# Performance work log

Measured on AMD Instinct MI355X. Metric: run time of the kernel, lower is better.

## Reference

```python
import jax, jax.numpy as jnp
import numpy as np

EPS_COS = 1e-8
EPS_NORM = 1e-12
LN_EPS = 1e-5
OT_REG = 0.05
OT_ITERS = 5

B, L, D_IN, D_H = 16, 512, 1024, 1024


def setup_inputs() -> dict:
    key = jax.random.key(0)
    ks = jax.random.split(key, 16)
    p = lambda k, shape: 0.02 * jax.random.normal(k, shape, dtype=jnp.float32)
    return {
        "origin_seq": jax.random.normal(ks[0], (B, L, D_IN), dtype=jnp.float32),
        "target_seq": jax.random.normal(ks[1], (B, L, D_IN), dtype=jnp.float32),
        "W_ori": p(ks[2], (D_IN, D_H)), "b_ori": jnp.zeros((D_H,), jnp.float32),
        "W_tar": p(ks[3], (D_IN, D_H)), "b_tar": jnp.zeros((D_H,), jnp.float32),
        "W_ft": p(ks[4], (D_H, D_H)), "b_ft": jnp.zeros((D_H,), jnp.float32),
        "W_fo": p(ks[5], (D_H, D_H)), "b_fo": jnp.zeros((D_H,), jnp.float32),
        "W_fot": p(ks[6], (D_H, D_H)), "b_fot": jnp.zeros((D_H,), jnp.float32),
        "ln_g": jnp.ones((D_H,), jnp.float32), "ln_b": jnp.zeros((D_H,), jnp.float32),
    }


def _l2norm(x, eps):
    return x / jnp.maximum(jnp.linalg.norm(x, axis=-1, keepdims=True), eps)


def _forward(origin_seq, target_seq, W_ori, b_ori, W_tar, b_tar, W_ft, b_ft,
             W_fo, b_fo, W_fot, b_fot, ln_g, ln_b):
    ori = origin_seq @ W_ori + b_ori            # [B, Lo, H]
    tar = target_seq @ W_tar + b_tar            # [B, Lt, H]
    tar = tar @ W_ft + b_ft
    ori_fc = ori @ W_fo + b_fo
    ori_tp = ori @ W_fot + b_fot
    # cosine similarity cost: [B, Lt, Lo]
    C = jnp.einsum('bth,boh->bto', _l2norm(tar, EPS_COS), _l2norm(ori_fc, EPS_COS))
    # Sinkhorn: alternating row/col normalization of exp(C/eps)
    Q = jnp.exp(C / OT_REG)
    for _ in range(OT_ITERS):
        Q = Q / jnp.sum(Q, axis=-1, keepdims=True)
        Q = Q / jnp.sum(Q, axis=-2, keepdims=True)
    plan = _l2norm(Q, EPS_NORM)                 # F.normalize(dim=-1); dropout is eval no-op
    out = jnp.einsum('bto,boh->bth', plan, ori_tp) + tar
    mu = jnp.mean(out, axis=-1, keepdims=True)
    var = jnp.mean((out - mu) ** 2, axis=-1, keepdims=True)
    return ((out - mu) * jax.lax.rsqrt(var + LN_EPS)) * ln_g + ln_b


def reference(origin_seq, target_seq, W_ori, b_ori, W_tar, b_tar, W_ft, b_ft,
              W_fo, b_fo, W_fot, b_fot, ln_g, ln_b):
    return _forward(origin_seq, target_seq, W_ori, b_ori, W_tar, b_tar, W_ft, b_ft,
                    W_fo, b_fo, W_fot, b_fot, ln_g, ln_b)
```

## Files before the change

### kernel.cpp

```cpp
#include <hip/hip_runtime.h>
#include <hip/hip_bf16.h>
#include <math.h>

constexpr int Bn = 16;
constexpr int Ln = 512;
constexpr int Hn = 1024;
constexpr int RowsT = Bn * Ln;

typedef __attribute__((ext_vector_type(8))) short bf16x8;
typedef __attribute__((ext_vector_type(4))) float f32x4;
typedef __attribute__((ext_vector_type(8))) unsigned short u16x8;

__device__ __forceinline__ unsigned short f2bf(float f) {
  unsigned u = __float_as_uint(f);
  u += 0x7FFFu + ((u >> 16) & 1u);
  return (unsigned short)(u >> 16);
}
__device__ __forceinline__ float bf2f(unsigned short u) {
  return __uint_as_float(((unsigned)u) << 16);
}

__device__ __forceinline__ void gload_lds16(const void* g, void* l) {
  __builtin_amdgcn_global_load_lds(
      (const __attribute__((address_space(1))) void*)g,
      (__attribute__((address_space(3))) void*)l, 16, 0, 0);
}

__device__ __forceinline__ float block_reduce_sum(float v) {
  __shared__ float sbuf[8];
  const int lane = threadIdx.x & 63;
  const int wid = threadIdx.x >> 6;
#pragma unroll
  for (int off = 32; off > 0; off >>= 1) v += __shfl_down(v, off, 64);
  __syncthreads();
  if (lane == 0) sbuf[wid] = v;
  __syncthreads();
  if (threadIdx.x == 0) {
    float t = 0.f;
    const int nw = (blockDim.x + 63) >> 6;
    for (int i = 0; i < nw; ++i) t += sbuf[i];
    sbuf[0] = t;
  }
  __syncthreads();
  return sbuf[0];
}

__global__ __launch_bounds__(256) void conv_z(
    const float* __restrict__ s0, const float* __restrict__ s1,
    unsigned short* __restrict__ d0, unsigned short* __restrict__ d1) {
  const float* in = blockIdx.z ? s1 : s0;
  unsigned short* out = blockIdx.z ? d1 : d0;
  const size_t i = ((size_t)blockIdx.x * blockDim.x + threadIdx.x) * 8;
  const float4 a = *(const float4*)(in + i);
  const float4 b = *(const float4*)(in + i + 4);
  u16x8 r;
  r[0] = f2bf(a.x); r[1] = f2bf(a.y); r[2] = f2bf(a.z); r[3] = f2bf(a.w);
  r[4] = f2bf(b.x); r[5] = f2bf(b.y); r[6] = f2bf(b.z); r[7] = f2bf(b.w);
  *(u16x8*)(out + i) = r;
}

__global__ __launch_bounds__(256) void transpose_w_z(
    const float* __restrict__ s0, const float* __restrict__ s1,
    unsigned short* __restrict__ d0, unsigned short* __restrict__ d1,
    int K, int N) {
  const float* W = blockIdx.z ? s1 : s0;
  unsigned short* Wt = blockIdx.z ? d1 : d0;
  __shared__ float t[32][33];
  const int n0 = blockIdx.x * 32;
  const int k0 = blockIdx.y * 32;
  const int tx = threadIdx.x & 31;
  const int ty = threadIdx.x >> 5;
#pragma unroll
  for (int i = 0; i < 32; i += 8)
    t[ty + i][tx] = W[(size_t)(k0 + ty + i) * N + n0 + tx];
  __syncthreads();
#pragma unroll
  for (int i = 0; i < 32; i += 8)
    Wt[(size_t)(n0 + ty + i) * K + k0 + tx] = f2bf(t[tx][ty + i]);
}

__global__ __launch_bounds__(256) void bias_combine(
    const float* __restrict__ b1a, const float* __restrict__ Wa, const float* __restrict__ b2a,
    const float* __restrict__ b1b, const float* __restrict__ Wb, const float* __restrict__ b2b,
    const float* __restrict__ b1c, const float* __restrict__ Wc, const float* __restrict__ b2c,
    float* __restrict__ o0, float* __restrict__ o1, float* __restrict__ o2) {
  const int z = blockIdx.y;
  const float* b1 = z == 0 ? b1a : (z == 1 ? b1b : b1c);
  const float* W  = z == 0 ? Wa  : (z == 1 ? Wb  : Wc);
  const float* b2 = z == 0 ? b2a : (z == 1 ? b2b : b2c);
  float* out      = z == 0 ? o0  : (z == 1 ? o1  : o2);
  const int n = blockIdx.x * 256 + threadIdx.x;
  float s = b2[n];
  for (int j = 0; j < Hn; ++j) s += b1[j] * W[(size_t)j * Hn + n];
  out[n] = s;
}

#define MFMA_PROLOG(Aptr, Bptr, Kdim)                                          \
  constexpr int BK = 32;                                                       \
  __shared__ unsigned short As[128][BK];                                       \
  __shared__ unsigned short Bs[128][BK];                                       \
  const int tid = threadIdx.x;                                                 \
  const int wid = tid >> 6;                                                    \
  const int lane = tid & 63;                                                   \
  const int wr = (wid >> 1) * 64;                                              \
  const int wc = (wid & 1) * 64;                                               \
  const int sr = lane >> 2;                                                    \
  const int sk = (lane & 3) * 8;                                               \
  const size_t arow = (size_t)(row0 + wid * 32 + sr) * Kdim + sk;              \
  const size_t brow = (size_t)(col0 + wid * 32 + sr) * Kdim + sk;              \
  f32x4 acc[4][4] = {};                                                        \
  for (int k0 = 0; k0 < Kdim; k0 += BK) {                                      \
    gload_lds16(Aptr + arow + k0,                      &As[wid * 32][0]);      \
    gload_lds16(Aptr + arow + (size_t)16 * Kdim + k0,  &As[wid * 32 + 16][0]); \
    gload_lds16(Bptr + brow + k0,                      &Bs[wid * 32][0]);      \
    gload_lds16(Bptr + brow + (size_t)16 * Kdim + k0,  &Bs[wid * 32 + 16][0]); \
    __syncthreads();                                                           \
    bf16x8 af[4], bfr[4];                                                      \
    _Pragma("unroll")                                                          \
    for (int m = 0; m < 4; ++m)                                                \
      af[m] = *(const bf16x8*)&As[wr + m * 16 + (lane & 15)][(lane >> 4) * 8]; \
    _Pragma("unroll")                                                          \
    for (int n = 0; n < 4; ++n)                                                \
      bfr[n] = *(const bf16x8*)&Bs[wc + n * 16 + (lane & 15)][(lane >> 4) * 8];\
    _Pragma("unroll")                                                          \
    for (int m = 0; m < 4; ++m)                                                \
      _Pragma("unroll")                                                        \
      for (int n = 0; n < 4; ++n)                                              \
        acc[m][n] = __builtin_amdgcn_mfma_f32_16x16x32_bf16(af[m], bfr[n],     \
                                                            acc[m][n], 0, 0, 0);\
    __syncthreads();                                                           \
  }                                                                            \
  const int cr = (lane >> 4) * 4;                                              \
  const int cc = lane & 15;

__global__ __launch_bounds__(256) void mfma_gemm_z(
    const unsigned short* __restrict__ A0, const unsigned short* __restrict__ A1,
    const unsigned short* __restrict__ Bt0, const unsigned short* __restrict__ Bt1,
    const float* __restrict__ bias0, const float* __restrict__ bias1,
    unsigned short* __restrict__ D0, unsigned short* __restrict__ D1,
    int mode1, int N, int K) {
  const int z = blockIdx.z;
  const unsigned short* A = z ? A1 : A0;
  const unsigned short* Bt = z ? Bt1 : Bt0;
  const float* bias = z ? bias1 : bias0;
  unsigned short* D = z ? D1 : D0;
  const int mode = z ? mode1 : 0;
  const int row0 = blockIdx.y * 128;
  const int col0 = blockIdx.x * 128;
  MFMA_PROLOG(A, Bt, K)
  if (mode == 0) {
#pragma unroll
    for (int m = 0; m < 4; ++m) {
#pragma unroll
      for (int n = 0; n < 4; ++n) {
        const int gc = col0 + wc + n * 16 + cc;
        const float bv = bias ? bias[gc] : 0.f;
#pragma unroll
        for (int r = 0; r < 4; ++r) {
          const int gr = row0 + wr + m * 16 + cr + r;
          D[(size_t)gr * N + gc] = f2bf(acc[m][n][r] + bv);
        }
      }
    }
  } else {
#pragma unroll
    for (int m = 0; m < 4; ++m) {
      const int gr0 = row0 + wr + m * 16 + cr;
      const int b = gr0 >> 9;
      const int o = gr0 & 511;
#pragma unroll
      for (int n = 0; n < 4; ++n) {
        const int gc = col0 + wc + n * 16 + cc;
        const float bv = bias ? bias[gc] : 0.f;
        ushort4 w;
        w.x = f2bf(acc[m][n][0] + bv);
        w.y = f2bf(acc[m][n][1] + bv);
        w.z = f2bf(acc[m][n][2] + bv);
        w.w = f2bf(acc[m][n][3] + bv);
        *(ushort4*)(D + ((size_t)b * Hn + gc) * Ln + o) = w;
      }
    }
  }
}

__global__ __launch_bounds__(256) void mfma_cos_exp(
    const unsigned short* __restrict__ TarBf, const unsigned short* __restrict__ FcBf,
    const float* __restrict__ rt, const float* __restrict__ rf,
    float* __restrict__ Q) {
  const int b = blockIdx.z;
  const unsigned short* Ab = TarBf + (size_t)b * Ln * Hn;
  const unsigned short* Bb = FcBf + (size_t)b * Ln * Hn;
  float* Qb = Q + (size_t)b * Ln * Ln;
  const int row0 = blockIdx.y * 128;
  const int col0 = blockIdx.x * 128;
  MFMA_PROLOG(Ab, Bb, Hn)
#pragma unroll
  for (int m = 0; m < 4; ++m) {
#pragma unroll
    for (int n = 0; n < 4; ++n) {
      const int o = col0 + wc + n * 16 + cc;
      const float rfo = rf[b * Ln + o] * 20.0f;
#pragma unroll
      for (int r = 0; r < 4; ++r) {
        const int t = row0 + wr + m * 16 + cr + r;
        const float c = acc[m][n][r] * rt[b * Ln + t] * rfo;
        Qb[(size_t)t * Ln + o] = __expf(c);
      }
    }
  }
}

__global__ __launch_bounds__(256) void mfma_out(
    const unsigned short* __restrict__ Plan, const unsigned short* __restrict__ TpT,
    const unsigned short* __restrict__ TarBf, float* __restrict__ Out) {
  const int b = blockIdx.z;
  const unsigned short* Ab = Plan + (size_t)b * Ln * Ln;
  const unsigned short* Bb = TpT + (size_t)b * Hn * Ln;
  const int row0 = blockIdx.y * 128;
  const int col0 = blockIdx.x * 128;
  MFMA_PROLOG(Ab, Bb, Ln)
#pragma unroll
  for (int m = 0; m < 4; ++m) {
#pragma unroll
    for (int n = 0; n < 4; ++n) {
      const int h = col0 + wc + n * 16 + cc;
#pragma unroll
      for (int r = 0; r < 4; ++r) {
        const int t = row0 + wr + m * 16 + cr + r;
        const size_t off = ((size_t)b * Ln + t) * Hn + h;
        Out[off] = acc[m][n][r] + bf2f(TarBf[off]);
      }
    }
  }
}

__global__ __launch_bounds__(256) void rownorm_z(
    const unsigned short* __restrict__ X0, const unsigned short* __restrict__ X1,
    float* __restrict__ r0, float* __restrict__ r1, float eps) {
  const unsigned short* X = blockIdx.y ? X1 : X0;
  float* r = blockIdx.y ? r1 : r0;
  const unsigned short* row = X + (size_t)blockIdx.x * Hn;
  const int i = threadIdx.x * 4;
  ushort4 v = *(const ushort4*)(row + i);
  float a0 = bf2f(v.x), a1 = bf2f(v.y), a2 = bf2f(v.z), a3 = bf2f(v.w);
  float s = block_reduce_sum(a0 * a0 + a1 * a1 + a2 * a2 + a3 * a3);
  if (threadIdx.x == 0) r[blockIdx.x] = 1.0f / fmaxf(sqrtf(s), eps);
}

template<bool FIRST>
__global__ __launch_bounds__(256) void u_step(
    const float* __restrict__ Q, const float* __restrict__ v, float* __restrict__ u) {
  const int row = blockIdx.x * 4 + (threadIdx.x >> 6);
  const int b = row >> 9;
  const int lane = threadIdx.x & 63;
  const float* q = Q + (size_t)row * Ln;
  const float4 a = *(const float4*)(q + lane * 8);
  const float4 c = *(const float4*)(q + lane * 8 + 4);
  float s;
  if (FIRST) {
    s = a.x + a.y + a.z + a.w + c.x + c.y + c.z + c.w;
  } else {
    const float* vb = v + b * Ln;
    const float4 va = *(const float4*)(vb + lane * 8);
    const float4 vc = *(const float4*)(vb + lane * 8 + 4);
    s = a.x * va.x + a.y * va.y + a.z * va.z + a.w * va.w +
        c.x * vc.x + c.y * vc.y + c.z * vc.z + c.w * vc.w;
  }
#pragma unroll
  for (int off = 32; off > 0; off >>= 1) s += __shfl_down(s, off, 64);
  if (lane == 0) u[row] = 1.0f / s;
}

__global__ __launch_bounds__(256) void v_step(
    const float* __restrict__ Q, const float* __restrict__ u, float* __restrict__ v) {
  const int b = blockIdx.y;
  const float* Qb = Q + (size_t)b * Ln * Ln;
  __shared__ float us[Ln];
  __shared__ float part[4][64];
  const int tid = threadIdx.x;
  us[tid] = u[b * Ln + tid];
  us[tid + 256] = u[b * Ln + tid + 256];
  __syncthreads();
  const int c = tid & 63;
  const int chunk = tid >> 6;
  const int o = blockIdx.x * 64 + c;
  float s = 0.f;
#pragma unroll 4
  for (int t = chunk * 128; t < chunk * 128 + 128; ++t)
    s += Qb[(size_t)t * Ln + o] * us[t];
  part[chunk][c] = s;
  __syncthreads();
  if (chunk == 0)
    v[b * Ln + o] = 1.0f / (part[0][c] + part[1][c] + part[2][c] + part[3][c]);
}

__global__ __launch_bounds__(256) void plan_prep(
    const float* __restrict__ Q, const float* __restrict__ v,
    unsigned short* __restrict__ P) {
  const int row = blockIdx.x;
  const int b = row >> 9;
  const float* q = Q + (size_t)row * Ln;
  const float* vb = v + b * Ln;
  const int i = threadIdx.x * 2;
  const float2 qq = *(const float2*)(q + i);
  const float2 vv = *(const float2*)(vb + i);
  const float p0 = qq.x * vv.x, p1 = qq.y * vv.y;
  const float s = block_reduce_sum(p0 * p0 + p1 * p1);
  const float rn = 1.0f / fmaxf(sqrtf(s), 1e-12f);
  ushort2 w;
  w.x = f2bf(p0 * rn);
  w.y = f2bf(p1 * rn);
  *(ushort2*)(P + (size_t)row * Ln + i) = w;
}

__global__ __launch_bounds__(256) void ln_kernel(
    float* __restrict__ Out, const float* __restrict__ g, const float* __restrict__ b) {
  float* row = Out + (size_t)blockIdx.x * Hn;
  const int tid = threadIdx.x;
  float4 v = reinterpret_cast<float4*>(row)[tid];
  float s = v.x + v.y + v.z + v.w;
  float ss = v.x * v.x + v.y * v.y + v.z * v.z + v.w * v.w;
  const float tot = block_reduce_sum(s);
  const float tot2 = block_reduce_sum(ss);
  const float mu = tot * (1.0f / Hn);
  const float var = tot2 * (1.0f / Hn) - mu * mu;
  const float rs = rsqrtf(var + 1e-5f);
  const float4 gg = reinterpret_cast<const float4*>(g)[tid];
  const float4 bb = reinterpret_cast<const float4*>(b)[tid];
  v.x = (v.x - mu) * rs * gg.x + bb.x;
  v.y = (v.y - mu) * rs * gg.y + bb.y;
  v.z = (v.z - mu) * rs * gg.z + bb.z;
  v.w = (v.w - mu) * rs * gg.w + bb.w;
  reinterpret_cast<float4*>(row)[tid] = v;
}

extern "C" void kernel_launch(void* const* d_in, const int* in_sizes, int n_in,
                              void* d_out, int out_size, void* d_ws, size_t ws_size,
                              hipStream_t stream) {
  const float* origin = (const float*)d_in[0];
  const float* target = (const float*)d_in[1];
  const float* W_ori = (const float*)d_in[2];
  const float* b_ori = (const float*)d_in[3];
  const float* W_tar = (const float*)d_in[4];
  const float* b_tar = (const float*)d_in[5];
  const float* W_ft = (const float*)d_in[6];
  const float* b_ft = (const float*)d_in[7];
  const float* W_fo = (const float*)d_in[8];
  const float* b_fo = (const float*)d_in[9];
  const float* W_fot = (const float*)d_in[10];
  const float* b_fot = (const float*)d_in[11];
  const float* ln_g = (const float*)d_in[12];
  const float* ln_b = (const float*)d_in[13];
  float* out = (float*)d_out;

  char* ws = (char*)d_ws;
  const size_t MB = 1048576;
  unsigned short* O_bf = (unsigned short*)(ws + 0);
  float* Qw = (float*)(ws + 0);
  unsigned short* T_bf = (unsigned short*)(ws + 16 * MB);
  unsigned short* Wori_bf = (unsigned short*)(ws + 16 * MB);
  unsigned short* WfoT = (unsigned short*)(ws + 18 * MB);
  unsigned short* WfotT = (unsigned short*)(ws + 20 * MB);
  unsigned short* Wc2T = (unsigned short*)(ws + 22 * MB);
  unsigned short* Wc3T = (unsigned short*)(ws + 24 * MB);
  unsigned short* plan_bf = (unsigned short*)(ws + 16 * MB);
  unsigned short* Wtar_bf = (unsigned short*)(ws + 32 * MB);
  unsigned short* WftT = (unsigned short*)(ws + 34 * MB);
  unsigned short* tar_bf = (unsigned short*)(ws + 32 * MB);
  unsigned short* Wc1T = (unsigned short*)(ws + 48 * MB);
  unsigned short* fc_bf = (unsigned short*)(ws + 48 * MB);
  unsigned short* tpT = (unsigned short*)(ws + 64 * MB);
  float* bc1 = (float*)(ws + 80 * MB);
  float* bc2 = bc1 + 1024;
  float* bc3 = bc2 + 1024;
  float* rt = bc3 + 1024;
  float* rf = rt + RowsT;
  float* uu = rf + RowsT;
  float* vv = uu + RowsT;

  const dim3 blk(256);

  conv_z<<<dim3(RowsT * Hn / 2048, 1, 2), blk, 0, stream>>>(origin, target, O_bf, T_bf);
  conv_z<<<dim3(Hn * Hn / 2048, 1, 1), blk, 0, stream>>>(W_tar, W_tar, Wtar_bf, Wtar_bf);
  transpose_w_z<<<dim3(32, 32, 1), blk, 0, stream>>>(W_ft, W_ft, WftT, WftT, Hn, Hn);
  bias_combine<<<dim3(4, 3), blk, 0, stream>>>(b_tar, W_ft, b_ft, b_ori, W_fo, b_fo,
                                               b_ori, W_fot, b_fot, bc1, bc2, bc3);
  mfma_gemm_z<<<dim3(8, 8, 1), blk, 0, stream>>>(WftT, WftT, Wtar_bf, Wtar_bf,
                                                 nullptr, nullptr, Wc1T, Wc1T, 0, Hn, Hn);
  mfma_gemm_z<<<dim3(8, 64, 1), blk, 0, stream>>>(T_bf, T_bf, Wc1T, Wc1T,
                                                  bc1, bc1, tar_bf, tar_bf, 0, Hn, Hn);
  conv_z<<<dim3(Hn * Hn / 2048, 1, 1), blk, 0, stream>>>(W_ori, W_ori, Wori_bf, Wori_bf);
  transpose_w_z<<<dim3(32, 32, 2), blk, 0, stream>>>(W_fo, W_fot, WfoT, WfotT, Hn, Hn);
  mfma_gemm_z<<<dim3(8, 8, 2), blk, 0, stream>>>(WfoT, WfotT, Wori_bf, Wori_bf,
                                                 nullptr, nullptr, Wc2T, Wc3T, 0, Hn, Hn);
  mfma_gemm_z<<<dim3(8, 64, 2), blk, 0, stream>>>(O_bf, O_bf, Wc2T, Wc3T,
                                                  bc2, bc3, fc_bf, tpT, 1, Hn, Hn);
  rownorm_z<<<dim3(RowsT, 2), blk, 0, stream>>>(tar_bf, fc_bf, rt, rf, 1e-8f);
  mfma_cos_exp<<<dim3(4, 4, Bn), blk, 0, stream>>>(tar_bf, fc_bf, rt, rf, Qw);
  u_step<true><<<dim3(RowsT / 4), blk, 0, stream>>>(Qw, vv, uu);
  v_step<<<dim3(Ln / 64, Bn), blk, 0, stream>>>(Qw, uu, vv);
  for (int it = 1; it < 5; ++it) {
    u_step<false><<<dim3(RowsT / 4), blk, 0, stream>>>(Qw, vv, uu);
    v_step<<<dim3(Ln / 64, Bn), blk, 0, stream>>>(Qw, uu, vv);
  }
  plan_prep<<<dim3(RowsT), blk, 0, stream>>>(Qw, vv, plan_bf);
  mfma_out<<<dim3(Hn / 128, Ln / 128, Bn), blk, 0, stream>>>(plan_bf, tpT, tar_bf, out);
  ln_kernel<<<dim3(RowsT), blk, 0, stream>>>(out, ln_g, ln_b);
}
```

Before: 487.9 us.

## Fuse Sinkhorn iterations into one per-batch kernel and merge projection GEMM launches

Replaces the ten separate u/v normalization launches and the plan_prep kernel with a single 1024-thread block per batch. That block keeps u and v in LDS and writes the normalized bf16 plan directly. The three weight-combine GEMMs are merged into one launch, and the three large activation GEMMs are merged into one 1D-grid kernel whose block index is remapped so that row tiles spread across XCDs. The conversion and transpose launches are also merged, and the workspace is relaid out to avoid aliasing. The aim is to remove launch overhead and intermediate u/v traffic. The cost is that the Sinkhorn stage runs on only 16 workgroups, so its bandwidth is limited to a small fraction of the CUs.

Result: no change. 479.6 us (-1.7%).

```diff
diff --git a/kernel.cpp b/kernel.cpp
--- a/kernel.cpp
+++ b/kernel.cpp
@@ -59,12 +59,13 @@
   *(u16x8*)(out + i) = r;
 }
 
-__global__ __launch_bounds__(256) void transpose_w_z(
-    const float* __restrict__ s0, const float* __restrict__ s1,
+__global__ __launch_bounds__(256) void transpose_w3(
+    const float* __restrict__ s0, const float* __restrict__ s1, const float* __restrict__ s2,
     unsigned short* __restrict__ d0, unsigned short* __restrict__ d1,
-    int K, int N) {
-  const float* W = blockIdx.z ? s1 : s0;
-  unsigned short* Wt = blockIdx.z ? d1 : d0;
+    unsigned short* __restrict__ d2, int K, int N) {
+  const int z = blockIdx.z;
+  const float* W = z == 0 ? s0 : (z == 1 ? s1 : s2);
+  unsigned short* Wt = z == 0 ? d0 : (z == 1 ? d1 : d2);
   __shared__ float t[32][33];
   const int n0 = blockIdx.x * 32;
   const int k0 = blockIdx.y * 32;
@@ -133,32 +134,67 @@
   const int cr = (lane >> 4) * 4;                                              \
   const int cc = lane & 15;
 
-__global__ __launch_bounds__(256) void mfma_gemm_z(
+__global__ __launch_bounds__(256) void mfma_gemm_w3(
     const unsigned short* __restrict__ A0, const unsigned short* __restrict__ A1,
-    const unsigned short* __restrict__ Bt0, const unsigned short* __restrict__ Bt1,
-    const float* __restrict__ bias0, const float* __restrict__ bias1,
+    const unsigned short* __restrict__ A2,
+    const unsigned short* __restrict__ B0, const unsigned short* __restrict__ B1,
+    const unsigned short* __restrict__ B2,
     unsigned short* __restrict__ D0, unsigned short* __restrict__ D1,
-    int mode1, int N, int K) {
+    unsigned short* __restrict__ D2, int N, int K) {
   const int z = blockIdx.z;
-  const unsigned short* A = z ? A1 : A0;
-  const unsigned short* Bt = z ? Bt1 : Bt0;
-  const float* bias = z ? bias1 : bias0;
-  unsigned short* D = z ? D1 : D0;
-  const int mode = z ? mode1 : 0;
+  const unsigned short* A = z == 0 ? A0 : (z == 1 ? A1 : A2);
+  const unsigned short* Bt = z == 0 ? B0 : (z == 1 ? B1 : B2);
+  unsigned short* D = z == 0 ? D0 : (z == 1 ? D1 : D2);
   const int row0 = blockIdx.y * 128;
   const int col0 = blockIdx.x * 128;
   MFMA_PROLOG(A, Bt, K)
-  if (mode == 0) {
+#pragma unroll
+  for (int m = 0; m < 4; ++m) {
+#pragma unroll
+    for (int n = 0; n < 4; ++n) {
+      const int gc = col0 + wc + n * 16 + cc;
+#pragma unroll
+      for (int r = 0; r < 4; ++r) {
+        const int gr = row0 + wr + m * 16 + cr + r;
+        D[(size_t)gr * N + gc] = f2bf(acc[m][n][r]);
+      }
+    }
+  }
+}
+
+__global__ __launch_bounds__(256) void mfma_gemm_big(
+    const unsigned short* __restrict__ Tb, const unsigned short* __restrict__ Ob,
+    const unsigned short* __restrict__ W1, const unsigned short* __restrict__ W2,
+    const unsigned short* __restrict__ W3,
+    const float* __restrict__ bc1, const float* __restrict__ bc2,
+    const float* __restrict__ bc3,
+    unsigned short* __restrict__ Dtar, unsigned short* __restrict__ Dfc,
+    unsigned short* __restrict__ DtpT) {
+  const int id = blockIdx.x;
+  const int xcd = id & 7;
+  const int j = id >> 3;
+  const int x = j & 7;
+  const int rest = j >> 3;
+  const int y = xcd + ((rest & 7) << 3);
+  const int z = rest >> 3;
+  const unsigned short* A = z == 0 ? Tb : Ob;
+  const unsigned short* Bt = z == 0 ? W1 : (z == 1 ? W2 : W3);
+  const float* bias = z == 0 ? bc1 : (z == 1 ? bc2 : bc3);
+  const int row0 = y * 128;
+  const int col0 = x * 128;
+  MFMA_PROLOG(A, Bt, Hn)
+  if (z != 2) {
+    unsigned short* D = z == 0 ? Dtar : Dfc;
 #pragma unroll
     for (int m = 0; m < 4; ++m) {
 #pragma unroll
       for (int n = 0; n < 4; ++n) {
         const int gc = col0 + wc + n * 16 + cc;
-        const float bv = bias ? bias[gc] : 0.f;
+        const float bv = bias[gc];
 #pragma unroll
         for (int r = 0; r < 4; ++r) {
           const int gr = row0 + wr + m * 16 + cr + r;
-          D[(size_t)gr * N + gc] = f2bf(acc[m][n][r] + bv);
+          D[(size_t)gr * Hn + gc] = f2bf(acc[m][n][r] + bv);
         }
       }
     }
@@ -171,13 +207,13 @@
 #pragma unroll
       for (int n = 0; n < 4; ++n) {
         const int gc = col0 + wc + n * 16 + cc;
-        const float bv = bias ? bias[gc] : 0.f;
+        const float bv = bias[gc];
         ushort4 w;
         w.x = f2bf(acc[m][n][0] + bv);
         w.y = f2bf(acc[m][n][1] + bv);
         w.z = f2bf(acc[m][n][2] + bv);
         w.w = f2bf(acc[m][n][3] + bv);
-        *(ushort4*)(D + ((size_t)b * Hn + gc) * Ln + o) = w;
+        *(ushort4*)(DtpT + ((size_t)b * Hn + gc) * Ln + o) = w;
       }
     }
   }
@@ -247,70 +283,64 @@
   if (threadIdx.x == 0) r[blockIdx.x] = 1.0f / fmaxf(sqrtf(s), eps);
 }
 
-template<bool FIRST>
-__global__ __launch_bounds__(256) void u_step(
-    const float* __restrict__ Q, const float* __restrict__ v, float* __restrict__ u) {
-  const int row = blockIdx.x * 4 + (threadIdx.x >> 6);
-  const int b = row >> 9;
-  const int lane = threadIdx.x & 63;
-  const float* q = Q + (size_t)row * Ln;
-  const float4 a = *(const float4*)(q + lane * 8);
-  const float4 c = *(const float4*)(q + lane * 8 + 4);
-  float s;
-  if (FIRST) {
-    s = a.x + a.y + a.z + a.w + c.x + c.y + c.z + c.w;
-  } else {
-    const float* vb = v + b * Ln;
-    const float4 va = *(const float4*)(vb + lane * 8);
-    const float4 vc = *(const float4*)(vb + lane * 8 + 4);
-    s = a.x * va.x + a.y * va.y + a.z * va.z + a.w * va.w +
-        c.x * vc.x + c.y * vc.y + c.z * vc.z + c.w * vc.w;
-  }
-#pragma unroll
-  for (int off = 32; off > 0; off >>= 1) s += __shfl_down(s, off, 64);
-  if (lane == 0) u[row] = 1.0f / s;
-}
-
-__global__ __launch_bounds__(256) void v_step(
-    const float* __restrict__ Q, const float* __restrict__ u, float* __restrict__ v) {
-  const int b = blockIdx.y;
+__global__ __launch_bounds__(1024) void sinkhorn_fused(
+    const float* __restrict__ Q, unsigned short* __restrict__ P) {
+  const int b = blockIdx.x;
   const float* Qb = Q + (size_t)b * Ln * Ln;
-  __shared__ float us[Ln];
-  __shared__ float part[4][64];
+  __shared__ __align__(16) float vsh[Ln];
+  __shared__ __align__(16) float ush[Ln];
+  __shared__ float part[1024];
   const int tid = threadIdx.x;
-  us[tid] = u[b * Ln + tid];
-  us[tid + 256] = u[b * Ln + tid + 256];
+  const int wv = tid >> 6;
+  const int lane = tid & 63;
+  const int o = tid & 511;
+  const int half = tid >> 9;
+  if (tid < Ln) vsh[tid] = 1.0f;
   __syncthreads();
-  const int c = tid & 63;
-  const int chunk = tid >> 6;
-  const int o = blockIdx.x * 64 + c;
-  float s = 0.f;
+  for (int it = 0; it < 5; ++it) {
+    for (int r = wv; r < Ln; r += 16) {
+      const float* q = Qb + (size_t)r * Ln;
+      const float4 a = *(const float4*)(q + lane * 8);
+      const float4 c = *(const float4*)(q + lane * 8 + 4);
+      const float4 va = *(const float4*)(vsh + lane * 8);
+      const float4 vc = *(const float4*)(vsh + lane * 8 + 4);
+      float s = a.x * va.x + a.y * va.y + a.z * va.z + a.w * va.w +
+                c.x * vc.x + c.y * vc.y + c.z * vc.z + c.w * vc.w;
+#pragma unroll
+      for (int off = 32; off > 0; off >>= 1) s += __shfl_down(s, off, 64);
+      if (lane == 0) ush[r] = 1.0f / s;
+    }
+    __syncthreads();
+    float s = 0.f;
+    const int t0 = half * 256;
 #pragma unroll 4
-  for (int t = chunk * 128; t < chunk * 128 + 128; ++t)
-    s += Qb[(size_t)t * Ln + o] * us[t];
-  part[chunk][c] = s;
-  __syncthreads();
-  if (chunk == 0)
-    v[b * Ln + o] = 1.0f / (part[0][c] + part[1][c] + part[2][c] + part[3][c]);
-}
-
-__global__ __launch_bounds__(256) void plan_prep(
-    const float* __restrict__ Q, const float* __restrict__ v,
-    unsigned short* __restrict__ P) {
-  const int row = blockIdx.x;
-  const int b = row >> 9;
-  const float* q = Q + (size_t)row * Ln;
-  const float* vb = v + b * Ln;
-  const int i = threadIdx.x * 2;
-  const float2 qq = *(const float2*)(q + i);
-  const float2 vv = *(const float2*)(vb + i);
-  const float p0 = qq.x * vv.x, p1 = qq.y * vv.y;
-  const float s = block_reduce_sum(p0 * p0 + p1 * p1);
-  const float rn = 1.0f / fmaxf(sqrtf(s), 1e-12f);
-  ushort2 w;
-  w.x = f2bf(p0 * rn);
-  w.y = f2bf(p1 * rn);
-  *(ushort2*)(P + (size_t)row * Ln + i) = w;
+    for (int t = t0; t < t0 + 256; ++t) s += Qb[(size_t)t * Ln + o] * ush[t];
+    part[tid] = s;
+    __syncthreads();
+    if (tid < Ln) vsh[tid] = 1.0f / (part[tid] + part[tid + 512]);
+    __syncthreads();
+  }
+  for (int r = wv; r < Ln; r += 16) {
+    const float* q = Qb + (size_t)r * Ln;
+    const float4 a = *(const float4*)(q + lane * 8);
+    const float4 c = *(const float4*)(q + lane * 8 + 4);
+    const float4 va = *(const float4*)(vsh + lane * 8);
+    const float4 vc = *(const float4*)(vsh + lane * 8 + 4);
+    float p[8];
+    p[0] = a.x * va.x; p[1] = a.y * va.y; p[2] = a.z * va.z; p[3] = a.w * va.w;
+    p[4] = c.x * vc.x; p[5] = c.y * vc.y; p[6] = c.z * vc.z; p[7] = c.w * vc.w;
+    float s = 0.f;
+#pragma unroll
+    for (int k = 0; k < 8; ++k) s += p[k] * p[k];
+#pragma unroll
+    for (int off = 32; off > 0; off >>= 1) s += __shfl_down(s, off, 64);
+    s = __shfl(s, 0, 64);
+    const float rn = 1.0f / fmaxf(sqrtf(s), 1e-12f);
+    u16x8 w;
+#pragma unroll
+    for (int k = 0; k < 8; ++k) w[k] = f2bf(p[k] * rn);
+    *(u16x8*)(P + ((size_t)b * Ln + r) * Ln + lane * 8) = w;
+  }
 }
 
 __global__ __launch_bounds__(256) void ln_kernel(
@@ -358,52 +388,40 @@
   unsigned short* O_bf = (unsigned short*)(ws + 0);
   float* Qw = (float*)(ws + 0);
   unsigned short* T_bf = (unsigned short*)(ws + 16 * MB);
-  unsigned short* Wori_bf = (unsigned short*)(ws + 16 * MB);
-  unsigned short* WfoT = (unsigned short*)(ws + 18 * MB);
-  unsigned short* WfotT = (unsigned short*)(ws + 20 * MB);
-  unsigned short* Wc2T = (unsigned short*)(ws + 22 * MB);
-  unsigned short* Wc3T = (unsigned short*)(ws + 24 * MB);
   unsigned short* plan_bf = (unsigned short*)(ws + 16 * MB);
-  unsigned short* Wtar_bf = (unsigned short*)(ws + 32 * MB);
-  unsigned short* WftT = (unsigned short*)(ws + 34 * MB);
   unsigned short* tar_bf = (unsigned short*)(ws + 32 * MB);
-  unsigned short* Wc1T = (unsigned short*)(ws + 48 * MB);
   unsigned short* fc_bf = (unsigned short*)(ws + 48 * MB);
   unsigned short* tpT = (unsigned short*)(ws + 64 * MB);
-  float* bc1 = (float*)(ws + 80 * MB);
+  unsigned short* Wc1T = (unsigned short*)(ws + 80 * MB);
+  unsigned short* Wc2T = (unsigned short*)(ws + 82 * MB);
+  unsigned short* Wc3T = (unsigned short*)(ws + 84 * MB);
+  unsigned short* Wtar_bf = (unsigned short*)(ws + 86 * MB);
+  unsigned short* Wori_bf = (unsigned short*)(ws + 88 * MB);
+  unsigned short* WftT = (unsigned short*)(ws + 90 * MB);
+  unsigned short* WfoT = (unsigned short*)(ws + 92 * MB);
+  unsigned short* WfotT = (unsigned short*)(ws + 94 * MB);
+  float* bc1 = (float*)(ws + 96 * MB);
   float* bc2 = bc1 + 1024;
   float* bc3 = bc2 + 1024;
   float* rt = bc3 + 1024;
   float* rf = rt + RowsT;
-  float* uu = rf + RowsT;
-  float* vv = uu + RowsT;
 
   const dim3 blk(256);
 
   conv_z<<<dim3(RowsT * Hn / 2048, 1, 2), blk, 0, stream>>>(origin, target, O_bf, T_bf);
-  conv_z<<<dim3(Hn * Hn / 2048, 1, 1), blk, 0, stream>>>(W_tar, W_tar, Wtar_bf, Wtar_bf);
-  transpose_w_z<<<dim3(32, 32, 1), blk, 0, stream>>>(W_ft, W_ft, WftT, WftT, Hn, Hn);
+  conv_z<<<dim3(Hn * Hn / 2048, 1, 2), blk, 0, stream>>>(W_tar, W_ori, Wtar_bf, Wori_bf);
+  transpose_w3<<<dim3(32, 32, 3), blk, 0, stream>>>(W_ft, W_fo, W_fot,
+                                                    WftT, WfoT, WfotT, Hn, Hn);
   bias_combine<<<dim3(4, 3), blk, 0, stream>>>(b_tar, W_ft, b_ft, b_ori, W_fo, b_fo,
                                                b_ori, W_fot, b_fot, bc1, bc2, bc3);
-  mfma_gemm_z<<<dim3(8, 8, 1), blk, 0, stream>>>(WftT, WftT, Wtar_bf, Wtar_bf,
-                                                 nullptr, nullptr, Wc1T, Wc1T, 0, Hn, Hn);
-  mfma_gemm_z<<<dim3(8, 64, 1), blk, 0, stream>>>(T_bf, T_bf, Wc1T, Wc1T,
-                                                  bc1, bc1, tar_bf, tar_bf, 0, Hn, Hn);
-  conv_z<<<dim3(Hn * Hn / 2048, 1, 1), blk, 0, stream>>>(W_ori, W_ori, Wori_bf, Wori_bf);
-  transpose_w_z<<<dim3(32, 32, 2), blk, 0, stream>>>(W_fo, W_fot, WfoT, WfotT, Hn, Hn);
-  mfma_gemm_z<<<dim3(8, 8, 2), blk, 0, stream>>>(WfoT, WfotT, Wori_bf, Wori_bf,
-                                                 nullptr, nullptr, Wc2T, Wc3T, 0, Hn, Hn);
-  mfma_gemm_z<<<dim3(8, 64, 2), blk, 0, stream>>>(O_bf, O_bf, Wc2T, Wc3T,
-                                                  bc2, bc3, fc_bf, tpT, 1, Hn, Hn);
+  mfma_gemm_w3<<<dim3(8, 8, 3), blk, 0, stream>>>(WftT, WfoT, WfotT,
+                                                  Wtar_bf, Wori_bf, Wori_bf,
+                                                  Wc1T, Wc2T, Wc3T, Hn, Hn);
+  mfma_gemm_big<<<dim3(1536), blk, 0, stream>>>(T_bf, O_bf, Wc1T, Wc2T, Wc3T,
+                                                bc1, bc2, bc3, tar_bf, fc_bf, tpT);
   rownorm_z<<<dim3(RowsT, 2), blk, 0, stream>>>(tar_bf, fc_bf, rt, rf, 1e-8f);
   mfma_cos_exp<<<dim3(4, 4, Bn), blk, 0, stream>>>(tar_bf, fc_bf, rt, rf, Qw);
-  u_step<true><<<dim3(RowsT / 4), blk, 0, stream>>>(Qw, vv, uu);
-  v_step<<<dim3(Ln / 64, Bn), blk, 0, stream>>>(Qw, uu, vv);
-  for (int it = 1; it < 5; ++it) {
-    u_step<false><<<dim3(RowsT / 4), blk, 0, stream>>>(Qw, vv, uu);
-    v_step<<<dim3(Ln / 64, Bn), blk, 0, stream>>>(Qw, uu, vv);
-  }
-  plan_prep<<<dim3(RowsT), blk, 0, stream>>>(Qw, vv, plan_bf);
+  sinkhorn_fused<<<dim3(Bn), dim3(1024), 0, stream>>>(Qw, plan_bf);
   mfma_out<<<dim3(Hn / 128, Ln / 128, Bn), blk, 0, stream>>>(plan_bf, tpT, tar_bf, out);
   ln_kernel<<<dim3(RowsT), blk, 0, stream>>>(out, ln_g, ln_b);
 }
```
